# Optimization experiments

Hardware: AMD Instinct MI355X
Metric: run time of the kernel (lower is better)

## Reference

```python
import jax, jax.numpy as jnp
import numpy as np

C_Z = 128
C_H = 128
N = 512
B = 1

def _layer_norm(x, g, b, eps=1e-5):
    mu = jnp.mean(x, axis=-1, keepdims=True)
    var = jnp.var(x, axis=-1, keepdims=True)
    return (x - mu) * jax.lax.rsqrt(var + eps) * g + b

def _linear(x, w, b):
    # torch Linear: y = x @ w.T + b, w: [out, in]
    return jnp.einsum('...i,oi->...o', x, w) + b

def setup_inputs() -> dict:
    key = jax.random.key(0)
    ks = jax.random.split(key, 8)
    s = 1.0 / np.sqrt(C_Z)
    return {
        'z': jax.random.normal(ks[0], (B, N, N, C_Z), jnp.float32),
        'mask': jnp.ones((B, N, N), jnp.float32),
        'ln_in_g': jnp.ones((C_Z,), jnp.float32),
        'ln_in_b': jnp.zeros((C_Z,), jnp.float32),
        'w_ag': jax.random.normal(ks[1], (C_H, C_Z), jnp.float32) * s,
        'b_ag': jnp.ones((C_H,), jnp.float32),
        'w_ap': jax.random.normal(ks[2], (C_H, C_Z), jnp.float32) * s,
        'b_ap': jnp.zeros((C_H,), jnp.float32),
        'w_bg': jax.random.normal(ks[3], (C_H, C_Z), jnp.float32) * s,
        'b_bg': jnp.ones((C_H,), jnp.float32),
        'w_bp': jax.random.normal(ks[4], (C_H, C_Z), jnp.float32) * s,
        'b_bp': jnp.zeros((C_H,), jnp.float32),
        'w_g': jax.random.normal(ks[5], (C_Z, C_Z), jnp.float32) * s,
        'b_g': jnp.zeros((C_Z,), jnp.float32),
        'w_z': jax.random.normal(ks[6], (C_Z, C_H), jnp.float32) * s,
        'b_z': jnp.zeros((C_Z,), jnp.float32),
        'ln_out_g': jnp.ones((C_H,), jnp.float32),
        'ln_out_b': jnp.zeros((C_H,), jnp.float32),
    }

def reference(z, mask, ln_in_g, ln_in_b, w_ag, b_ag, w_ap, b_ap,
              w_bg, b_bg, w_bp, b_bp, w_g, b_g, w_z, b_z,
              ln_out_g, ln_out_b):
    m = mask[..., None]                       # [B,N,N,1]
    zn = _layer_norm(z, ln_in_g, ln_in_b)     # [B,N,N,Cz]
    a = m * jax.nn.sigmoid(_linear(zn, w_ag, b_ag)) * _linear(zn, w_ap, b_ap)
    b = m * jax.nn.sigmoid(_linear(zn, w_bg, b_bg)) * _linear(zn, w_bp, b_bp)
    # outgoing: x[b,i,j,c] = sum_k a[b,i,k,c] * b[b,j,k,c]
    x = jnp.einsum('bikc,bjkc->bijc', a, b)
    x = _layer_norm(x, ln_out_g, ln_out_b)
    x = _linear(x, w_z, b_z)
    g = jax.nn.sigmoid(_linear(zn, w_g, b_g))
    return x * g
```

## Files before the change

### kernel.cpp

```cpp
#include <hip/hip_runtime.h>

#define NN 512
#define CCH 128
#define MM (NN*NN)

using f32x4  = __attribute__((ext_vector_type(4))) float;
using f32x2  = __attribute__((ext_vector_type(2))) float;
using bf16x8 = __attribute__((ext_vector_type(8))) short;
using u16x4  = __attribute__((ext_vector_type(4))) unsigned short;
using u32x2  = __attribute__((ext_vector_type(2))) unsigned int;
using u32x4  = __attribute__((ext_vector_type(4))) unsigned int;
typedef unsigned short u16;

__device__ __forceinline__ u16 f2bf(float f) {
    unsigned u = __builtin_bit_cast(unsigned, f);
    u += 0x7FFF + ((u >> 16) & 1);
    return (u16)(u >> 16);
}
__device__ __forceinline__ float bf2f(u16 h) {
    unsigned u = ((unsigned)h) << 16;
    return __builtin_bit_cast(float, u);
}
__device__ __forceinline__ unsigned pack2(float lo, float hi) {
    return (unsigned)f2bf(lo) | ((unsigned)f2bf(hi) << 16);
}
__device__ __forceinline__ float sigm(float x) { return 1.0f / (1.0f + __expf(-x)); }

__device__ __forceinline__ void gl_lds16(const void* g, void* l) {
    __builtin_amdgcn_global_load_lds(
        (const __attribute__((address_space(1))) void*)g,
        (__attribute__((address_space(3))) void*)l, 16, 0, 0);
}

__global__ __launch_bounds__(256) void k_prep(
    const float* __restrict__ w0, const float* __restrict__ w1,
    const float* __restrict__ w2, const float* __restrict__ w3,
    const float* __restrict__ w4, const float* __restrict__ w5,
    const float* __restrict__ b0, const float* __restrict__ b1,
    const float* __restrict__ b2, const float* __restrict__ b3,
    const float* __restrict__ b4, const float* __restrict__ b5,
    const float* __restrict__ gin, const float* __restrict__ bin,
    const float* __restrict__ gout, const float* __restrict__ bout,
    u16* __restrict__ wbf, float* __restrict__ bias2) {
    int mat = blockIdx.x;
    const float* W = mat==0?w0:mat==1?w1:mat==2?w2:mat==3?w3:mat==4?w4:w5;
    const float* B = mat==0?b0:mat==1?b1:mat==2?b2:mat==3?b3:mat==4?b4:b5;
    const float* G = (mat==5)? gout : gin;
    const float* Bt= (mat==5)? bout : bin;
    __shared__ float gs[CCH], bs[CCH];
    int tid = threadIdx.x;
    if (tid < CCH) { gs[tid] = G[tid]; bs[tid] = Bt[tid]; }
    __syncthreads();
    int o = tid >> 1, c0 = (tid & 1) * 64;
    const float* src = W + o * CCH + c0;
    char* dstrow = (char*)(wbf + mat * 16384) + o * 256;
    int key = o & 7;
    float dot = 0.f;
    #pragma unroll
    for (int q = 0; q < 16; ++q) {
        f32x4 v = *(const f32x4*)(src + q * 4);
        int c = c0 + q * 4;
        dot += bs[c]*v.x + bs[c+1]*v.y + bs[c+2]*v.z + bs[c+3]*v.w;
        u16x4 p;
        p.x = f2bf(v.x * gs[c]);     p.y = f2bf(v.y * gs[c+1]);
        p.z = f2bf(v.z * gs[c+2]);   p.w = f2bf(v.w * gs[c+3]);
        int chunk = (c0 >> 3) + (q >> 1);
        *(u16x4*)(dstrow + (((chunk ^ key)) << 4) + ((q & 1) << 3)) = p;
    }
    dot += __shfl_xor(dot, 1);
    if ((tid & 1) == 0) bias2[mat * CCH + o] = B[o] + dot;
}

__global__ __launch_bounds__(512, 4) void k_fused(
    const float* __restrict__ z, const float* __restrict__ mask,
    const u16* __restrict__ wbf, const float* __restrict__ bias2,
    u16* __restrict__ aT, u16* __restrict__ bT, u16* gateB) {
    __shared__ __align__(16) u16 wls[32768];
    int tid = threadIdx.x, w = tid >> 6, lane = tid & 63;
    int r = lane & 15, kq = lane >> 4;
    long m0 = (long)blockIdx.x * 128;

    {
        const char* Wg = (const char*)wbf;
        #pragma unroll
        for (int it = 0; it < 8; ++it)
            gl_lds16(Wg + (long)it * 8192 + tid * 16, (char*)wls + it * 8192 + w * 1024);
    }

    long mrow = m0 + w * 16 + r;
    bf16x8 av[4];
    {
        const float* zr = z + mrow * CCH;
        f32x4 zv[4][2];
        float s = 0.f, s2 = 0.f;
        #pragma unroll
        for (int kb = 0; kb < 4; ++kb) {
            zv[kb][0] = *(const f32x4*)(zr + kb * 32 + kq * 8);
            zv[kb][1] = *(const f32x4*)(zr + kb * 32 + kq * 8 + 4);
            #pragma unroll
            for (int h = 0; h < 2; ++h) {
                f32x4 v = zv[kb][h];
                s += v.x + v.y + v.z + v.w;
                s2 = fmaf(v.x, v.x, fmaf(v.y, v.y, fmaf(v.z, v.z, fmaf(v.w, v.w, s2))));
            }
        }
        s  += __shfl_xor(s, 16);  s  += __shfl_xor(s, 32);
        s2 += __shfl_xor(s2, 16); s2 += __shfl_xor(s2, 32);
        float mu = s * (1.0f / CCH);
        float var = fmaxf(s2 * (1.0f / CCH) - mu * mu, 0.f);
        float rs = rsqrtf(var + 1e-5f);
        #pragma unroll
        for (int kb = 0; kb < 4; ++kb) {
            f32x4 a0 = zv[kb][0], a1 = zv[kb][1];
            u32x4 o;
            o[0] = pack2((a0.x - mu) * rs, (a0.y - mu) * rs);
            o[1] = pack2((a0.z - mu) * rs, (a0.w - mu) * rs);
            o[2] = pack2((a1.x - mu) * rs, (a1.y - mu) * rs);
            o[3] = pack2((a1.z - mu) * rs, (a1.w - mu) * rs);
            av[kb] = __builtin_bit_cast(bf16x8, o);
        }
    }
    f32x4 mkv = *(const f32x4*)(mask + m0 + w * 16 + kq * 4);

    __syncthreads();

    int i7 = (int)((blockIdx.x >> 2) & 7);
    int q = w * 2 + (kq >> 1);
    long boff = m0 * 2 + ((long)(q >> 3) << 7) + ((long)((q & 7) ^ i7) << 4)
              + ((kq & 1) << 3);

    #pragma unroll 1
    for (int ph = 0; ph < 2; ++ph) {
        if (ph == 1) {
            __syncthreads();
            const char* Wg = (const char*)wbf + 65536;
            #pragma unroll
            for (int it = 0; it < 8; ++it)
                gl_lds16(Wg + (long)it * 8192 + tid * 16, (char*)wls + it * 8192 + w * 1024);
            __syncthreads();
        }
        const float* B1 = bias2 + (ph * 2) * CCH;
        const float* B2 = bias2 + (ph * 2 + 1) * CCH;
        f32x4 acc1[8], acc2[8];
        #pragma unroll
        for (int nt = 0; nt < 8; ++nt) { acc1[nt] = {0,0,0,0}; acc2[nt] = {0,0,0,0}; }
        #pragma unroll
        for (int nt = 0; nt < 8; ++nt) {
            int ol = nt * 16 + r;
            int key = ol & 7;
            const char* row1 = (const char*)wls + ol * 256;
            const char* row2 = (const char*)wls + 32768 + ol * 256;
            #pragma unroll
            for (int kb = 0; kb < 4; ++kb) {
                int ph16 = ((kb * 4 + kq) ^ key) << 4;
                bf16x8 b1 = *(const bf16x8*)(row1 + ph16);
                bf16x8 b2 = *(const bf16x8*)(row2 + ph16);
                acc1[nt] = __builtin_amdgcn_mfma_f32_16x16x32_bf16(av[kb], b1, acc1[nt], 0, 0, 0);
                acc2[nt] = __builtin_amdgcn_mfma_f32_16x16x32_bf16(av[kb], b2, acc2[nt], 0, 0, 0);
            }
        }
        u16* dst = ph ? bT : aT;
        #pragma unroll
        for (int nt = 0; nt < 8; ++nt) {
            int cc = nt * 16 + r;
            float b1v = B1[cc], b2v = B2[cc];
            float v0 = mkv[0] * sigm(acc1[nt][0] + b1v) * (acc2[nt][0] + b2v);
            float v1 = mkv[1] * sigm(acc1[nt][1] + b1v) * (acc2[nt][1] + b2v);
            float v2 = mkv[2] * sigm(acc1[nt][2] + b1v) * (acc2[nt][2] + b2v);
            float v3 = mkv[3] * sigm(acc1[nt][3] + b1v) * (acc2[nt][3] + b2v);
            u32x2 pv; pv.x = pack2(v0, v1); pv.y = pack2(v2, v3);
            *(u32x2*)((char*)dst + ((long)cc << 19) + boff) = pv;
        }
    }

    __syncthreads();
    {
        const char* Wg = (const char*)wbf + 131072;
        #pragma unroll
        for (int it = 0; it < 4; ++it)
            gl_lds16(Wg + (long)it * 8192 + tid * 16, (char*)wls + it * 8192 + w * 1024);
    }
    __syncthreads();
    {
        f32x4 acc[8];
        #pragma unroll
        for (int nt = 0; nt < 8; ++nt) acc[nt] = {0,0,0,0};
        #pragma unroll
        for (int nt = 0; nt < 8; ++nt) {
            int ol = nt * 16 + r;
            int key = ol & 7;
            const char* row1 = (const char*)wls + ol * 256;
            #pragma unroll
            for (int kb = 0; kb < 4; ++kb) {
                bf16x8 b1 = *(const bf16x8*)(row1 + (((kb * 4 + kq) ^ key) << 4));
                acc[nt] = __builtin_amdgcn_mfma_f32_16x16x32_bf16(b1, av[kb], acc[nt], 0, 0, 0);
            }
        }
        #pragma unroll
        for (int nt = 0; nt < 8; ++nt) {
            int c0 = nt * 16 + kq * 4;
            f32x4 bg = *(const f32x4*)(bias2 + 4 * CCH + c0);
            u32x2 pv;
            pv.x = pack2(sigm(acc[nt][0] + bg[0]), sigm(acc[nt][1] + bg[1]));
            pv.y = pack2(sigm(acc[nt][2] + bg[2]), sigm(acc[nt][3] + bg[3]));
            *(u32x2*)(gateB + mrow * 256 + c0) = pv;
        }
    }
}

__global__ __launch_bounds__(256, 4) void k_tri(const u16* __restrict__ aT,
                                                const u16* __restrict__ bT,
                                                u16* __restrict__ xT) {
    __shared__ __align__(16) char shm[34816];
    u16* At = (u16*)shm;
    u16* Bt = (u16*)(shm + 16384);
    int tid = threadIdx.x;
    int w = tid >> 6, lane = tid & 63;
    int r = lane & 15, kq = lane >> 4;

    int L = blockIdx.x;
    int xcd = L & 7, idx = L >> 3;
    int c    = xcd + 8 * (idx >> 4);
    int tile = idx & 15;
    int ti = tile >> 2, tj = tile & 3;

    const char* abase = (const char*)(aT + (long)c * MM) + (long)(ti * 128) * 1024;
    const char* bbase = (const char*)(bT + (long)c * MM) + (long)(tj * 128) * 1024;
    int wm = w >> 1, wn = w & 1;

    f32x4 acc[4][4];
    #pragma unroll
    for (int a = 0; a < 4; ++a)
        #pragma unroll
        for (int bq = 0; bq < 4; ++bq) acc[a][bq] = {0.f,0.f,0.f,0.f};

    for (int ks = 0; ks < 8; ++ks) {
        const char* asrc = abase + ks * 128;
        const char* bsrc = bbase + ks * 128;
        #pragma unroll
        for (int it = 0; it < 4; ++it) {
            int u = it * 256 + tid;
            long goff = (long)(u >> 3) * 1024 + (u & 7) * 16;
            gl_lds16(asrc + goff, (char*)At + it * 4096 + w * 1024);
            gl_lds16(bsrc + goff, (char*)Bt + it * 4096 + w * 1024);
        }
        __syncthreads();

        #pragma unroll
        for (int kh = 0; kh < 2; ++kh) {
            bf16x8 af[4];
            #pragma unroll
            for (int mt = 0; mt < 4; ++mt) {
                int rowa = wm * 64 + mt * 16 + r;
                af[mt] = *(const bf16x8*)((const char*)At + rowa * 128 +
                                          (((kh * 4 + kq) ^ (r & 7)) << 4));
            }
            #pragma unroll
            for (int nt = 0; nt < 4; ++nt) {
                int rowb = wn * 64 + nt * 16 + r;
                bf16x8 bf = *(const bf16x8*)((const char*)Bt + rowb * 128 +
                                             (((kh * 4 + kq) ^ (r & 7)) << 4));
                #pragma unroll
                for (int mt = 0; mt < 4; ++mt)
                    acc[mt][nt] = __builtin_amdgcn_mfma_f32_16x16x32_bf16(bf, af[mt], acc[mt][nt], 0, 0, 0);
            }
        }
        __syncthreads();
    }

    char* tb = shm;
    #pragma unroll
    for (int mt = 0; mt < 4; ++mt) {
        int il = wm * 64 + mt * 16 + r;
        #pragma unroll
        for (int nt = 0; nt < 4; ++nt) {
            int jl = wn * 64 + nt * 16 + kq * 4;
            u32x2 pv;
            pv.x = pack2(acc[mt][nt][0], acc[mt][nt][1]);
            pv.y = pack2(acc[mt][nt][2], acc[mt][nt][3]);
            *(u32x2*)(tb + il * 272 + jl * 2) = pv;
        }
    }
    __syncthreads();
    u16* xrow = xT + (long)c * MM + (long)(ti * 128) * NN + tj * 128;
    int joff = tid & 15;
    #pragma unroll
    for (int rd = 0; rd < 8; ++rd) {
        int il = rd * 16 + (tid >> 4);
        u32x4 vv = *(const u32x4*)(tb + il * 272 + joff * 16);
        *(u32x4*)(xrow + (long)il * NN + joff * 8) = vv;
    }
}

__global__ __launch_bounds__(256, 4) void k_out(const u16* __restrict__ xT,
                                                const u16* __restrict__ wbf,
                                                const float* __restrict__ bias2,
                                                const u16* gateB,
                                                float* __restrict__ outp) {
    __shared__ __align__(16) u16 xl[64 * 128];
    int tid = threadIdx.x, w = tid >> 6, lane = tid & 63;
    int r = lane & 15, kq = lane >> 4;
    long m0 = (long)blockIdx.x * 64;

    {
        int cg = tid & 31, ms = tid >> 5;
        int c0 = cg * 4;
        const u16* base = xT + m0 + (long)ms * 8;
        bf16x8 v0 = *(const bf16x8*)(base + (long)(c0 + 0) * MM);
        bf16x8 v1 = *(const bf16x8*)(base + (long)(c0 + 1) * MM);
        bf16x8 v2 = *(const bf16x8*)(base + (long)(c0 + 2) * MM);
        bf16x8 v3 = *(const bf16x8*)(base + (long)(c0 + 3) * MM);
        #pragma unroll
        for (int e = 0; e < 8; ++e) {
            int m = ms * 8 + e;
            u16x4 t;
            t.x = (u16)v0[e]; t.y = (u16)v1[e]; t.z = (u16)v2[e]; t.w = (u16)v3[e];
            *(u16x4*)((char*)xl + m * 256 + ((c0 * 2) ^ ((m & 15) << 4))) = t;
        }
    }
    __syncthreads();

    int mlr = w * 16 + r;
    int swm = (mlr & 15) << 4;
    u32x4 avu[4];
    float s = 0.f, s2 = 0.f;
    #pragma unroll
    for (int kb = 0; kb < 4; ++kb) {
        avu[kb] = *(const u32x4*)((const char*)xl + mlr * 256 + ((kb * 64 + kq * 16) ^ swm));
        #pragma unroll
        for (int p = 0; p < 4; ++p) {
            unsigned u = avu[kb][p];
            float flo = __builtin_bit_cast(float, u << 16);
            float fhi = __builtin_bit_cast(float, u & 0xFFFF0000u);
            s += flo + fhi;
            s2 = fmaf(flo, flo, s2);
            s2 = fmaf(fhi, fhi, s2);
        }
    }
    s  += __shfl_xor(s, 16);  s  += __shfl_xor(s, 32);
    s2 += __shfl_xor(s2, 16); s2 += __shfl_xor(s2, 32);
    float mu = s * (1.0f / CCH);
    float var = fmaxf(s2 * (1.0f / CCH) - mu * mu, 0.f);
    float rs = rsqrtf(var + 1e-5f);
    float nmu = -mu * rs;
    bf16x8 av[4];
    #pragma unroll
    for (int kb = 0; kb < 4; ++kb) {
        u32x4 o;
        #pragma unroll
        for (int p = 0; p < 4; ++p) {
            unsigned u = avu[kb][p];
            float flo = __builtin_bit_cast(float, u << 16);
            float fhi = __builtin_bit_cast(float, u & 0xFFFF0000u);
            o[p] = pack2(fmaf(flo, rs, nmu), fmaf(fhi, rs, nmu));
        }
        av[kb] = __builtin_bit_cast(bf16x8, o);
    }

    long m = m0 + w * 16 + r;
    u16x4 gvu[8];
    #pragma unroll
    for (int nt = 0; nt < 8; ++nt)
        gvu[nt] = *(const u16x4*)(gateB + m * 256 + nt * 16 + kq * 4);

    const char* Wz = (const char*)(wbf + 5 * 16384);
    f32x4 acc[8];
    #pragma unroll
    for (int nt = 0; nt < 8; ++nt) acc[nt] = {0,0,0,0};
    #pragma unroll
    for (int nt = 0; nt < 8; ++nt) {
        int ol = nt * 16 + r;
        int key = ol & 7;
        const char* row = Wz + ol * 256;
        #pragma unroll
        for (int kb = 0; kb < 4; ++kb) {
            bf16x8 bw = *(const bf16x8*)(row + (((kb * 4 + kq) ^ key) << 4));
            acc[nt] = __builtin_amdgcn_mfma_f32_16x16x32_bf16(bw, av[kb], acc[nt], 0, 0, 0);
        }
    }

    __syncthreads();

    const float* b2z = bias2 + 5 * CCH;
    #pragma unroll
    for (int nt = 0; nt < 8; ++nt) {
        int c0 = nt * 16 + kq * 4;
        f32x4 bb = *(const f32x4*)(b2z + c0);
        f32x4 o;
        #pragma unroll
        for (int j = 0; j < 4; ++j)
            o[j] = (acc[nt][j] + bb[j]) * bf2f(gvu[nt][j]);
        *(f32x4*)(outp + m * CCH + c0) = o;
    }
}

extern "C" void kernel_launch(void* const* d_in, const int* in_sizes, int n_in,
                              void* d_out, int out_size, void* d_ws, size_t ws_size,
                              hipStream_t stream) {
    const float* z       = (const float*)d_in[0];
    const float* mask    = (const float*)d_in[1];
    const float* ln_in_g = (const float*)d_in[2];
    const float* ln_in_b = (const float*)d_in[3];
    const float* w_ag    = (const float*)d_in[4];
    const float* b_ag    = (const float*)d_in[5];
    const float* w_ap    = (const float*)d_in[6];
    const float* b_ap    = (const float*)d_in[7];
    const float* w_bg    = (const float*)d_in[8];
    const float* b_bg    = (const float*)d_in[9];
    const float* w_bp    = (const float*)d_in[10];
    const float* b_bp    = (const float*)d_in[11];
    const float* w_g     = (const float*)d_in[12];
    const float* b_g     = (const float*)d_in[13];
    const float* w_z     = (const float*)d_in[14];
    const float* b_z     = (const float*)d_in[15];
    const float* ln_o_g  = (const float*)d_in[16];
    const float* ln_o_b  = (const float*)d_in[17];
    float* out = (float*)d_out;
    u16* gateB = (u16*)d_out;

    char* ws = (char*)d_ws;
    const size_t SL = (size_t)MM * CCH * 2;
    u16* xT   = (u16*)ws;
    u16* aT   = (u16*)(ws + SL);
    u16* bT   = (u16*)(ws + 2 * SL);
    u16* wbf  = (u16*)(ws + 3 * SL);
    float* b2 = (float*)(ws + 3 * SL + 6 * 16384 * 2);

    k_prep<<<6, 256, 0, stream>>>(w_ag, w_ap, w_bg, w_bp, w_g, w_z,
                                  b_ag, b_ap, b_bg, b_bp, b_g, b_z,
                                  ln_in_g, ln_in_b, ln_o_g, ln_o_b, wbf, b2);
    k_fused<<<MM / 128, 512, 0, stream>>>(z, mask, wbf, b2, aT, bT, gateB);
    k_tri<<<2048, 256, 0, stream>>>(aT, bT, xT);
    k_out<<<MM / 64, 256, 0, stream>>>(xT, wbf, b2, gateB, out);
}
```

Before: 311.3 us.

## Process two row tiles per block in k_fused and overlap weight loads with epilogues

The projection kernel now handles 256 rows per block instead of 128, so each LDS-staged weight fragment feeds two row tiles and the per-block weight-load cost is spread over twice as many rows. The gate and projection MFMA work is split into column halves so the next weight matrix can be loaded into LDS while the epilogue of the previous half runs. k_out also hoists its bias loads ahead of the GEMM. In exchange the grid has half as many blocks, and the extra accumulators and activations raise register pressure, which could reduce occupancy under the 512-thread, 4-block launch bound.

```diff
diff --git a/kernel.cpp b/kernel.cpp
--- a/kernel.cpp
+++ b/kernel.cpp
@@ -78,7 +78,7 @@
     __shared__ __align__(16) u16 wls[32768];
     int tid = threadIdx.x, w = tid >> 6, lane = tid & 63;
     int r = lane & 15, kq = lane >> 4;
-    long m0 = (long)blockIdx.x * 128;
+    long m0 = (long)blockIdx.x * 256;
 
     {
         const char* Wg = (const char*)wbf;
@@ -87,10 +87,10 @@
             gl_lds16(Wg + (long)it * 8192 + tid * 16, (char*)wls + it * 8192 + w * 1024);
     }
 
-    long mrow = m0 + w * 16 + r;
-    bf16x8 av[4];
-    {
-        const float* zr = z + mrow * CCH;
+    bf16x8 av[2][4];
+    #pragma unroll
+    for (int t = 0; t < 2; ++t) {
+        const float* zr = z + (m0 + t * 128 + w * 16 + r) * CCH;
         f32x4 zv[4][2];
         float s = 0.f, s2 = 0.f;
         #pragma unroll
@@ -117,62 +117,82 @@
             o[1] = pack2((a0.z - mu) * rs, (a0.w - mu) * rs);
             o[2] = pack2((a1.x - mu) * rs, (a1.y - mu) * rs);
             o[3] = pack2((a1.z - mu) * rs, (a1.w - mu) * rs);
-            av[kb] = __builtin_bit_cast(bf16x8, o);
-        }
-    }
-    f32x4 mkv = *(const f32x4*)(mask + m0 + w * 16 + kq * 4);
-
-    __syncthreads();
-
-    int i7 = (int)((blockIdx.x >> 2) & 7);
+            av[t][kb] = __builtin_bit_cast(bf16x8, o);
+        }
+    }
+    f32x4 mkv[2];
+    mkv[0] = *(const f32x4*)(mask + m0 + w * 16 + kq * 4);
+    mkv[1] = *(const f32x4*)(mask + m0 + 128 + w * 16 + kq * 4);
+
+    int i7 = (int)((blockIdx.x >> 1) & 7);
     int q = w * 2 + (kq >> 1);
-    long boff = m0 * 2 + ((long)(q >> 3) << 7) + ((long)((q & 7) ^ i7) << 4)
-              + ((kq & 1) << 3);
-
-    #pragma unroll 1
-    for (int ph = 0; ph < 2; ++ph) {
-        if (ph == 1) {
-            __syncthreads();
-            const char* Wg = (const char*)wbf + 65536;
-            #pragma unroll
-            for (int it = 0; it < 8; ++it)
-                gl_lds16(Wg + (long)it * 8192 + tid * 16, (char*)wls + it * 8192 + w * 1024);
-            __syncthreads();
-        }
-        const float* B1 = bias2 + (ph * 2) * CCH;
-        const float* B2 = bias2 + (ph * 2 + 1) * CCH;
-        f32x4 acc1[8], acc2[8];
-        #pragma unroll
-        for (int nt = 0; nt < 8; ++nt) { acc1[nt] = {0,0,0,0}; acc2[nt] = {0,0,0,0}; }
-        #pragma unroll
-        for (int nt = 0; nt < 8; ++nt) {
-            int ol = nt * 16 + r;
+    long bo_base = ((long)(q >> 3) << 7) + ((long)((q & 7) ^ i7) << 4) + ((kq & 1) << 3);
+    long boff0 = m0 * 2 + bo_base;
+    long boff1 = (m0 + 128) * 2 + bo_base;
+
+    f32x4 acc1[2][4], acc2[2][4];
+
+    auto mfma_half = [&](int nb) {
+        #pragma unroll
+        for (int tt = 0; tt < 2; ++tt)
+            #pragma unroll
+            for (int nt = 0; nt < 4; ++nt) { acc1[tt][nt] = {0,0,0,0}; acc2[tt][nt] = {0,0,0,0}; }
+        #pragma unroll
+        for (int nt = 0; nt < 4; ++nt) {
+            int ol = (nb + nt) * 16 + r;
             int key = ol & 7;
             const char* row1 = (const char*)wls + ol * 256;
-            const char* row2 = (const char*)wls + 32768 + ol * 256;
+            const char* row2 = row1 + 32768;
             #pragma unroll
             for (int kb = 0; kb < 4; ++kb) {
                 int ph16 = ((kb * 4 + kq) ^ key) << 4;
                 bf16x8 b1 = *(const bf16x8*)(row1 + ph16);
                 bf16x8 b2 = *(const bf16x8*)(row2 + ph16);
-                acc1[nt] = __builtin_amdgcn_mfma_f32_16x16x32_bf16(av[kb], b1, acc1[nt], 0, 0, 0);
-                acc2[nt] = __builtin_amdgcn_mfma_f32_16x16x32_bf16(av[kb], b2, acc2[nt], 0, 0, 0);
-            }
-        }
-        u16* dst = ph ? bT : aT;
-        #pragma unroll
-        for (int nt = 0; nt < 8; ++nt) {
-            int cc = nt * 16 + r;
-            float b1v = B1[cc], b2v = B2[cc];
-            float v0 = mkv[0] * sigm(acc1[nt][0] + b1v) * (acc2[nt][0] + b2v);
-            float v1 = mkv[1] * sigm(acc1[nt][1] + b1v) * (acc2[nt][1] + b2v);
-            float v2 = mkv[2] * sigm(acc1[nt][2] + b1v) * (acc2[nt][2] + b2v);
-            float v3 = mkv[3] * sigm(acc1[nt][3] + b1v) * (acc2[nt][3] + b2v);
-            u32x2 pv; pv.x = pack2(v0, v1); pv.y = pack2(v2, v3);
-            *(u32x2*)((char*)dst + ((long)cc << 19) + boff) = pv;
-        }
-    }
-
+                acc1[0][nt] = __builtin_amdgcn_mfma_f32_16x16x32_bf16(av[0][kb], b1, acc1[0][nt], 0, 0, 0);
+                acc1[1][nt] = __builtin_amdgcn_mfma_f32_16x16x32_bf16(av[1][kb], b1, acc1[1][nt], 0, 0, 0);
+                acc2[0][nt] = __builtin_amdgcn_mfma_f32_16x16x32_bf16(av[0][kb], b2, acc2[0][nt], 0, 0, 0);
+                acc2[1][nt] = __builtin_amdgcn_mfma_f32_16x16x32_bf16(av[1][kb], b2, acc2[1][nt], 0, 0, 0);
+            }
+        }
+    };
+    auto epi_half = [&](u16* dst, int nb, int mat1) {
+        #pragma unroll
+        for (int nt = 0; nt < 4; ++nt) {
+            int cc = (nb + nt) * 16 + r;
+            float bb1 = bias2[mat1 * CCH + cc];
+            float bb2 = bias2[(mat1 + 1) * CCH + cc];
+            long plane = (long)cc << 19;
+            #pragma unroll
+            for (int t = 0; t < 2; ++t) {
+                f32x4 a1 = acc1[t][nt], a2 = acc2[t][nt];
+                float v0 = mkv[t][0] * sigm(a1[0] + bb1) * (a2[0] + bb2);
+                float v1 = mkv[t][1] * sigm(a1[1] + bb1) * (a2[1] + bb2);
+                float v2 = mkv[t][2] * sigm(a1[2] + bb1) * (a2[2] + bb2);
+                float v3 = mkv[t][3] * sigm(a1[3] + bb1) * (a2[3] + bb2);
+                u32x2 pv; pv.x = pack2(v0, v1); pv.y = pack2(v2, v3);
+                *(u32x2*)((char*)dst + plane + (t ? boff1 : boff0)) = pv;
+            }
+        }
+    };
+
+    __syncthreads();
+
+    mfma_half(0);
+    epi_half(aT, 0, 0);
+    mfma_half(4);
+    __syncthreads();
+    {
+        const char* Wg = (const char*)wbf + 65536;
+        #pragma unroll
+        for (int it = 0; it < 8; ++it)
+            gl_lds16(Wg + (long)it * 8192 + tid * 16, (char*)wls + it * 8192 + w * 1024);
+    }
+    epi_half(aT, 4, 0);
+    __syncthreads();
+
+    mfma_half(0);
+    epi_half(bT, 0, 2);
+    mfma_half(4);
     __syncthreads();
     {
         const char* Wg = (const char*)wbf + 131072;
@@ -180,30 +200,40 @@
         for (int it = 0; it < 4; ++it)
             gl_lds16(Wg + (long)it * 8192 + tid * 16, (char*)wls + it * 8192 + w * 1024);
     }
-    __syncthreads();
-    {
-        f32x4 acc[8];
-        #pragma unroll
-        for (int nt = 0; nt < 8; ++nt) acc[nt] = {0,0,0,0};
-        #pragma unroll
-        for (int nt = 0; nt < 8; ++nt) {
-            int ol = nt * 16 + r;
+    epi_half(bT, 4, 2);
+    __syncthreads();
+
+    #pragma unroll
+    for (int nb = 0; nb < 8; nb += 4) {
+        f32x4 ga[2][4];
+        #pragma unroll
+        for (int tt = 0; tt < 2; ++tt)
+            #pragma unroll
+            for (int nt = 0; nt < 4; ++nt) ga[tt][nt] = {0,0,0,0};
+        #pragma unroll
+        for (int nt = 0; nt < 4; ++nt) {
+            int ol = (nb + nt) * 16 + r;
             int key = ol & 7;
             const char* row1 = (const char*)wls + ol * 256;
             #pragma unroll
             for (int kb = 0; kb < 4; ++kb) {
                 bf16x8 b1 = *(const bf16x8*)(row1 + (((kb * 4 + kq) ^ key) << 4));
-                acc[nt] = __builtin_amdgcn_mfma_f32_16x16x32_bf16(b1, av[kb], acc[nt], 0, 0, 0);
-            }
-        }
-        #pragma unroll
-        for (int nt = 0; nt < 8; ++nt) {
-            int c0 = nt * 16 + kq * 4;
+                ga[0][nt] = __builtin_amdgcn_mfma_f32_16x16x32_bf16(b1, av[0][kb], ga[0][nt], 0, 0, 0);
+                ga[1][nt] = __builtin_amdgcn_mfma_f32_16x16x32_bf16(b1, av[1][kb], ga[1][nt], 0, 0, 0);
+            }
+        }
+        #pragma unroll
+        for (int nt = 0; nt < 4; ++nt) {
+            int c0 = (nb + nt) * 16 + kq * 4;
             f32x4 bg = *(const f32x4*)(bias2 + 4 * CCH + c0);
-            u32x2 pv;
-            pv.x = pack2(sigm(acc[nt][0] + bg[0]), sigm(acc[nt][1] + bg[1]));
-            pv.y = pack2(sigm(acc[nt][2] + bg[2]), sigm(acc[nt][3] + bg[3]));
-            *(u32x2*)(gateB + mrow * 256 + c0) = pv;
+            #pragma unroll
+            for (int t = 0; t < 2; ++t) {
+                long m = m0 + t * 128 + w * 16 + r;
+                u32x2 pv;
+                pv.x = pack2(sigm(ga[t][nt][0] + bg[0]), sigm(ga[t][nt][1] + bg[1]));
+                pv.y = pack2(sigm(ga[t][nt][2] + bg[2]), sigm(ga[t][nt][3] + bg[3]));
+                *(u32x2*)(gateB + m * 256 + c0) = pv;
+            }
         }
     }
 }
@@ -359,9 +389,12 @@
 
     long m = m0 + w * 16 + r;
     u16x4 gvu[8];
-    #pragma unroll
-    for (int nt = 0; nt < 8; ++nt)
+    f32x4 bb[8];
+    #pragma unroll
+    for (int nt = 0; nt < 8; ++nt) {
         gvu[nt] = *(const u16x4*)(gateB + m * 256 + nt * 16 + kq * 4);
+        bb[nt]  = *(const f32x4*)(bias2 + 5 * CCH + nt * 16 + kq * 4);
+    }
 
     const char* Wz = (const char*)(wbf + 5 * 16384);
     f32x4 acc[8];
@@ -381,15 +414,13 @@
 
     __syncthreads();
 
-    const float* b2z = bias2 + 5 * CCH;
     #pragma unroll
     for (int nt = 0; nt < 8; ++nt) {
         int c0 = nt * 16 + kq * 4;
-        f32x4 bb = *(const f32x4*)(b2z + c0);
         f32x4 o;
         #pragma unroll
         for (int j = 0; j < 4; ++j)
-            o[j] = (acc[nt][j] + bb[j]) * bf2f(gvu[nt][j]);
+            o[j] = (acc[nt][j] + bb[nt][j]) * bf2f(gvu[nt][j]);
         *(f32x4*)(outp + m * CCH + c0) = o;
     }
 }
@@ -429,7 +460,7 @@
     k_prep<<<6, 256, 0, stream>>>(w_ag, w_ap, w_bg, w_bp, w_g, w_z,
                                   b_ag, b_ap, b_bg, b_bp, b_g, b_z,
                                   ln_in_g, ln_in_b, ln_o_g, ln_o_b, wbf, b2);
-    k_fused<<<MM / 128, 512, 0, stream>>>(z, mask, wbf, b2, aT, bT, gateB);
+    k_fused<<<MM / 256, 512, 0, stream>>>(z, mask, wbf, b2, aT, bT, gateB);
     k_tri<<<2048, 256, 0, stream>>>(aT, bT, xT);
     k_out<<<MM / 64, 256, 0, stream>>>(xT, wbf, b2, gateB, out);
 }
```

Result: slower. 370.2 us (+18.9%).
